# Performance work log

Measured on AMD Instinct MI355X. Metric: run time of the kernel, lower is better.

The kernel has to match this reference:

```python
import jax, jax.numpy as jnp
import numpy as np

X_DIM = 512
HID = 1024


def setup_inputs() -> dict:
    key = jax.random.key(0)
    ks = jax.random.split(key, 9)
    X = jax.random.normal(ks[0], (64, 512, X_DIM), dtype=jnp.float32)
    def w(k, shape):
        return jax.random.normal(k, shape, dtype=jnp.float32) * 0.1
    return {
        "X": X,
        "W_hi": w(ks[1], (HID, HID)), "W_xi": w(ks[2], (X_DIM, HID)), "b_i": jnp.zeros((HID,), jnp.float32),
        "W_hf": w(ks[3], (HID, HID)), "W_xf": w(ks[4], (X_DIM, HID)), "b_f": jnp.zeros((HID,), jnp.float32),
        "W_ho": w(ks[5], (HID, HID)), "W_xo": w(ks[6], (X_DIM, HID)), "b_o": jnp.zeros((HID,), jnp.float32),
        "W_hz": w(ks[7], (HID, HID)), "W_xz": w(ks[8], (X_DIM, HID)), "b_z": jnp.zeros((HID,), jnp.float32),
    }


def reference(X, W_hi, W_xi, b_i, W_hf, W_xf, b_f, W_ho, W_xo, b_o, W_hz, W_xz, b_z):
    B, T, _ = X.shape
    H = W_hi.shape[0]
    # Precompute input projections for all timesteps in one batched GEMM each
    # (same math as per-step x @ W_x*): [B,T,4H]
    Wx = jnp.concatenate([W_xi, W_xf, W_xo, W_xz], axis=1)   # [x_dim, 4H]
    Wh = jnp.concatenate([W_hi, W_hf, W_ho, W_hz], axis=1)   # [H, 4H]
    b = jnp.concatenate([b_i, b_f, b_o, b_z])                # [4H]
    xproj = jnp.einsum('btd,dg->btg', X, Wx) + b             # [B,T,4H]

    def step(carry, xp):
        h, c = carry
        g = h @ Wh + xp                                      # [B,4H]
        i = jax.nn.sigmoid(g[:, 0*H:1*H])
        f = jax.nn.sigmoid(g[:, 1*H:2*H])
        o = jax.nn.sigmoid(g[:, 2*H:3*H])
        z = jnp.tanh(g[:, 3*H:4*H])
        c = i * z + f * c
        h = o * jnp.tanh(c)
        return (h, c), h

    h0 = jnp.zeros((B, H), X.dtype)
    c0 = jnp.zeros((B, H), X.dtype)
    _, hs = jax.lax.scan(step, (h0, c0), jnp.swapaxes(xproj, 0, 1))  # hs: [T,B,H]
    return jnp.swapaxes(hs, 0, 1)                            # [B,T,H]
```

## Files before the change

### kernel.cpp

```cpp
#include <hip/hip_runtime.h>

#define TT 512
#define XD 512
#define HH 1024
#define NGROUP 4
#define BLK_PER_G 64
#define MROWS 16

#define GRP_DW 8192

typedef __attribute__((ext_vector_type(8))) _Float16 h8;
typedef __attribute__((ext_vector_type(4))) float f4;

__global__ __launch_bounds__(256, 1) void lstm_fused(
    const float* __restrict__ X,
    const float* __restrict__ Whi, const float* __restrict__ Wxi, const float* __restrict__ bi_p,
    const float* __restrict__ Whf, const float* __restrict__ Wxf, const float* __restrict__ bf_p,
    const float* __restrict__ Who, const float* __restrict__ Wxo, const float* __restrict__ bo_p,
    const float* __restrict__ Whz, const float* __restrict__ Wxz, const float* __restrict__ bz_p,
    float* __restrict__ out,
    int* __restrict__ flags,
    int* __restrict__ hxch)
{
    __shared__ float red[3][4][2][64][2];
    __shared__ _Float16 sh16[16][16];

    const int tid  = threadIdx.x;
    const int wave = tid >> 6;
    const int lane = tid & 63;
    const int ln   = lane & 15;
    const int lq   = lane >> 4;

    const int blk = blockIdx.x;
    const int g   = blk & 3;
    const int j   = blk >> 2;
    const int colbase = j * 16;
    const int rowbase = g * MROWS;
    const int col = colbase + ln;

    const float* Wh[4]   = {Whi, Whf, Who, Whz};
    const float* Wx[4]   = {Wxi, Wxf, Wxo, Wxz};
    const float* bias[4] = {bi_p, bf_p, bo_p, bz_p};

    h8 bh[4][8];
    h8 bx[4][4];
#pragma unroll
    for (int gi = 0; gi < 4; ++gi) {
        const float* W = Wh[gi];
#pragma unroll
        for (int kt = 0; kt < 8; ++kt) {
            const int k0 = wave * 256 + kt * 32 + lq * 8;
            h8 f;
#pragma unroll
            for (int q = 0; q < 8; ++q) f[q] = (_Float16)W[(k0 + q) * HH + col];
            bh[gi][kt] = f;
        }
        const float* Wq = Wx[gi];
#pragma unroll
        for (int kt = 0; kt < 4; ++kt) {
            const int k0 = wave * 128 + kt * 32 + lq * 8;
            h8 f;
#pragma unroll
            for (int q = 0; q < 8; ++q) f[q] = (_Float16)Wq[(k0 + q) * HH + col];
            bx[gi][kt] = f;
        }
    }
    float bsum[4];
#pragma unroll
    for (int gi = 0; gi < 4; ++gi) bsum[gi] = bias[gi][col];

    float cprev[4] = {0.f, 0.f, 0.f, 0.f};

    const float* Xrow = X + (size_t)(rowbase + ln) * (TT * XD);
    const int xbase = g * GRP_DW;

    for (int t = 0; t < TT; ++t) {
        h8 ax[4];
#pragma unroll
        for (int kt = 0; kt < 4; ++kt) {
            const float4* xp = (const float4*)(Xrow + t * XD + wave * 128 + kt * 32 + lq * 8);
            float4 a = xp[0], b2 = xp[1];
            h8 f;
            f[0] = (_Float16)a.x;  f[1] = (_Float16)a.y;
            f[2] = (_Float16)a.z;  f[3] = (_Float16)a.w;
            f[4] = (_Float16)b2.x; f[5] = (_Float16)b2.y;
            f[6] = (_Float16)b2.z; f[7] = (_Float16)b2.w;
            ax[kt] = f;
        }

        f4 acc[4];
#pragma unroll
        for (int gi = 0; gi < 4; ++gi) acc[gi] = (f4){0.f, 0.f, 0.f, 0.f};

#pragma unroll
        for (int kt = 0; kt < 4; ++kt)
#pragma unroll
            for (int gi = 0; gi < 4; ++gi)
                acc[gi] = __builtin_amdgcn_mfma_f32_16x16x32_f16(ax[kt], bx[gi][kt], acc[gi], 0, 0, 0);

        if (t > 0) {
            int* fl = flags + g * BLK_PER_G;
            while (true) {
                int v = __hip_atomic_load(fl + lane, __ATOMIC_RELAXED, __HIP_MEMORY_SCOPE_AGENT);
                if (__all(v >= t)) break;
                __builtin_amdgcn_s_sleep(1);
            }
            asm volatile("" ::: "memory");

            const int rb = ((t - 1) & 1) * (NGROUP * GRP_DW) + xbase;
            h8 ah[8];
#pragma unroll
            for (int kt = 0; kt < 8; ++kt) {
                const int dwi = rb + ((wave * 32 + kt * 4 + lq) * 16 + ln) * 4;
                union { int i[4]; h8 f; } u;
                u.i[0] = __hip_atomic_load(hxch + dwi + 0, __ATOMIC_RELAXED, __HIP_MEMORY_SCOPE_AGENT);
                u.i[1] = __hip_atomic_load(hxch + dwi + 1, __ATOMIC_RELAXED, __HIP_MEMORY_SCOPE_AGENT);
                u.i[2] = __hip_atomic_load(hxch + dwi + 2, __ATOMIC_RELAXED, __HIP_MEMORY_SCOPE_AGENT);
                u.i[3] = __hip_atomic_load(hxch + dwi + 3, __ATOMIC_RELAXED, __HIP_MEMORY_SCOPE_AGENT);
                ah[kt] = u.f;
            }
#pragma unroll
            for (int kt = 0; kt < 8; ++kt)
#pragma unroll
                for (int gi = 0; gi < 4; ++gi)
                    acc[gi] = __builtin_amdgcn_mfma_f32_16x16x32_f16(ah[kt], bh[gi][kt], acc[gi], 0, 0, 0);
        }

        if (wave > 0) {
#pragma unroll
            for (int gi = 0; gi < 4; ++gi) {
                red[wave - 1][gi][0][lane][0] = acc[gi][0];
                red[wave - 1][gi][0][lane][1] = acc[gi][1];
                red[wave - 1][gi][1][lane][0] = acc[gi][2];
                red[wave - 1][gi][1][lane][1] = acc[gi][3];
            }
        }
        __syncthreads();

        if (wave == 0) {
#pragma unroll
            for (int w = 0; w < 3; ++w)
#pragma unroll
                for (int gi = 0; gi < 4; ++gi) {
                    acc[gi][0] += red[w][gi][0][lane][0];
                    acc[gi][1] += red[w][gi][0][lane][1];
                    acc[gi][2] += red[w][gi][1][lane][0];
                    acc[gi][3] += red[w][gi][1][lane][1];
                }

#pragma unroll
            for (int r = 0; r < 4; ++r) {
                float gi_ = acc[0][r] + bsum[0];
                float gf_ = acc[1][r] + bsum[1];
                float go_ = acc[2][r] + bsum[2];
                float gz_ = acc[3][r] + bsum[3];
                float i_ = 1.f / (1.f + __expf(-gi_));
                float f_ = 1.f / (1.f + __expf(-gf_));
                float o_ = 1.f / (1.f + __expf(-go_));
                float z_ = 1.f - 2.f / (__expf(2.f * gz_) + 1.f);
                float c_ = i_ * z_ + f_ * cprev[r];
                cprev[r] = c_;
                float h_ = o_ * (1.f - 2.f / (__expf(2.f * c_) + 1.f));
                const int m = lq * 4 + r;
                out[(size_t)(rowbase + m) * (TT * HH) + (size_t)t * HH + col] = h_;
                sh16[m][ln] = (_Float16)h_;
            }

            asm volatile("s_waitcnt lgkmcnt(0)" ::: "memory");
            if (lane < 32) {
                const int prow = lane & 15;
                const int pk8  = lane >> 4;
                const int4 pk = *(const int4*)&sh16[prow][pk8 * 8];
                const int wb = (t & 1) * (NGROUP * GRP_DW) + xbase
                             + ((j * 2 + pk8) * 16 + prow) * 4;
                __hip_atomic_store(hxch + wb + 0, pk.x, __ATOMIC_RELAXED, __HIP_MEMORY_SCOPE_AGENT);
                __hip_atomic_store(hxch + wb + 1, pk.y, __ATOMIC_RELAXED, __HIP_MEMORY_SCOPE_AGENT);
                __hip_atomic_store(hxch + wb + 2, pk.z, __ATOMIC_RELAXED, __HIP_MEMORY_SCOPE_AGENT);
                __hip_atomic_store(hxch + wb + 3, pk.w, __ATOMIC_RELAXED, __HIP_MEMORY_SCOPE_AGENT);
            }
            asm volatile("s_waitcnt vmcnt(0)" ::: "memory");
            if (lane == 0) {
                __hip_atomic_store(&flags[g * BLK_PER_G + j], t + 1,
                                   __ATOMIC_RELAXED, __HIP_MEMORY_SCOPE_AGENT);
            }
        }
    }
}

extern "C" void kernel_launch(void* const* d_in, const int* in_sizes, int n_in,
                              void* d_out, int out_size, void* d_ws, size_t ws_size,
                              hipStream_t stream) {
    const float* X   = (const float*)d_in[0];
    const float* Whi = (const float*)d_in[1];
    const float* Wxi = (const float*)d_in[2];
    const float* bi  = (const float*)d_in[3];
    const float* Whf = (const float*)d_in[4];
    const float* Wxf = (const float*)d_in[5];
    const float* bf  = (const float*)d_in[6];
    const float* Who = (const float*)d_in[7];
    const float* Wxo = (const float*)d_in[8];
    const float* bo  = (const float*)d_in[9];
    const float* Whz = (const float*)d_in[10];
    const float* Wxz = (const float*)d_in[11];
    const float* bz  = (const float*)d_in[12];
    float* out = (float*)d_out;

    int* flags = (int*)d_ws;
    int* hxch  = flags + 256;
    hipMemsetAsync(d_ws, 0, NGROUP * BLK_PER_G * sizeof(int), stream);

    lstm_fused<<<dim3(256), dim3(256), 0, stream>>>(
        X, Whi, Wxi, bi, Whf, Wxf, bf, Who, Wxo, bo, Whz, Wxz, bz, out, flags, hxch);
}
```

Measured before the change: 3.084 ms.

## Split LSTM gate epilogue across two waves and prefetch next-step X inputs

Moves the flag poll and h-exchange loads to the start of each step, so the X-projection MFMAs no longer sit on the critical path after the wait. The next step's X rows are prefetched into registers during the current step. The gate reduction and activations are split across two waves, with a shared-memory token so that all h stores finish before the flag is published. Exchange loads and stores are widened to 64-bit atomics and each wave polls only 16 flags. The cost is an LDS spin between waves and more registers held for prefetched data.

Result: slower. 3.838 ms (+24.4%).

```diff
diff --git a/kernel.cpp b/kernel.cpp
--- a/kernel.cpp
+++ b/kernel.cpp
@@ -5,12 +5,15 @@
 #define HH 1024
 #define NGROUP 4
 #define BLK_PER_G 64
-#define MROWS 16
-
 #define GRP_DW 8192
 
 typedef __attribute__((ext_vector_type(8))) _Float16 h8;
 typedef __attribute__((ext_vector_type(4))) float f4;
+typedef __attribute__((ext_vector_type(4))) int i4;
+typedef unsigned long long u64;
+
+__device__ __forceinline__ float sigf(float x) { return 1.f / (1.f + __expf(-x)); }
+__device__ __forceinline__ float tanhfast(float x) { return 1.f - 2.f / (__expf(2.f * x) + 1.f); }
 
 __global__ __launch_bounds__(256, 1) void lstm_fused(
     const float* __restrict__ X,
@@ -22,8 +25,9 @@
     int* __restrict__ flags,
     int* __restrict__ hxch)
 {
-    __shared__ float red[3][4][2][64][2];
-    __shared__ _Float16 sh16[16][16];
+    __shared__ f4 red[4][4][64];
+    __shared__ __align__(16) _Float16 sh16[16][16];
+    __shared__ int stoken;
 
     const int tid  = threadIdx.x;
     const int wave = tid >> 6;
@@ -35,8 +39,10 @@
     const int g   = blk & 3;
     const int j   = blk >> 2;
     const int colbase = j * 16;
-    const int rowbase = g * MROWS;
+    const int rowbase = g * 16;
     const int col = colbase + ln;
+
+    if (tid == 0) stoken = 0;
 
     const float* Wh[4]   = {Whi, Whf, Who, Whz};
     const float* Wx[4]   = {Wxi, Wxf, Wxo, Wxz};
@@ -69,17 +75,52 @@
 #pragma unroll
     for (int gi = 0; gi < 4; ++gi) bsum[gi] = bias[gi][col];
 
-    float cprev[4] = {0.f, 0.f, 0.f, 0.f};
+    const int m0 = (wave & 1) * 8 + lq * 2;
+    const int m1 = m0 + 1;
+    float cp0 = 0.f, cp1 = 0.f;
 
     const float* Xrow = X + (size_t)(rowbase + ln) * (TT * XD);
-    const int xbase = g * GRP_DW;
+    const int gbase = g * GRP_DW;
+
+    const int* fp = flags + g * BLK_PER_G + ((lane < 16) ? (wave * 16 + lane) : j);
+
+    float4 xv[8];
+    {
+        const float* xb = Xrow + wave * 128;
+#pragma unroll
+        for (int kt = 0; kt < 4; ++kt) {
+            const float4* xp = (const float4*)(xb + kt * 32 + lq * 8);
+            xv[2 * kt] = xp[0]; xv[2 * kt + 1] = xp[1];
+        }
+    }
+    __syncthreads();
+
+    u64 hv[8][2];
 
     for (int t = 0; t < TT; ++t) {
+        if (t > 0) {
+            while (true) {
+                int v = __hip_atomic_load(fp, __ATOMIC_RELAXED, __HIP_MEMORY_SCOPE_AGENT);
+                if (__all(v >= t)) break;
+                __builtin_amdgcn_s_sleep(1);
+            }
+            const int rb = ((t - 1) & 1) * (NGROUP * GRP_DW) + gbase;
+#pragma unroll
+            for (int kt = 0; kt < 8; ++kt) {
+                const u64* hp = (const u64*)(hxch + rb + ((wave * 32 + kt * 4 + lq) * 16 + ln) * 4);
+                hv[kt][0] = __hip_atomic_load(hp + 0, __ATOMIC_RELAXED, __HIP_MEMORY_SCOPE_AGENT);
+                hv[kt][1] = __hip_atomic_load(hp + 1, __ATOMIC_RELAXED, __HIP_MEMORY_SCOPE_AGENT);
+            }
+        }
+
+        f4 acc[4];
+#pragma unroll
+        for (int gi = 0; gi < 4; ++gi) acc[gi] = (f4){0.f, 0.f, 0.f, 0.f};
+
         h8 ax[4];
 #pragma unroll
         for (int kt = 0; kt < 4; ++kt) {
-            const float4* xp = (const float4*)(Xrow + t * XD + wave * 128 + kt * 32 + lq * 8);
-            float4 a = xp[0], b2 = xp[1];
+            float4 a = xv[2 * kt], b2 = xv[2 * kt + 1];
             h8 f;
             f[0] = (_Float16)a.x;  f[1] = (_Float16)a.y;
             f[2] = (_Float16)a.z;  f[3] = (_Float16)a.w;
@@ -87,11 +128,6 @@
             f[6] = (_Float16)b2.z; f[7] = (_Float16)b2.w;
             ax[kt] = f;
         }
-
-        f4 acc[4];
-#pragma unroll
-        for (int gi = 0; gi < 4; ++gi) acc[gi] = (f4){0.f, 0.f, 0.f, 0.f};
-
 #pragma unroll
         for (int kt = 0; kt < 4; ++kt)
 #pragma unroll
@@ -99,89 +135,87 @@
                 acc[gi] = __builtin_amdgcn_mfma_f32_16x16x32_f16(ax[kt], bx[gi][kt], acc[gi], 0, 0, 0);
 
         if (t > 0) {
-            int* fl = flags + g * BLK_PER_G;
-            while (true) {
-                int v = __hip_atomic_load(fl + lane, __ATOMIC_RELAXED, __HIP_MEMORY_SCOPE_AGENT);
-                if (__all(v >= t)) break;
-                __builtin_amdgcn_s_sleep(1);
+#pragma unroll
+            for (int kt = 0; kt < 8; ++kt) {
+                union { u64 u[2]; h8 f; } uu;
+                uu.u[0] = hv[kt][0]; uu.u[1] = hv[kt][1];
+#pragma unroll
+                for (int gi = 0; gi < 4; ++gi)
+                    acc[gi] = __builtin_amdgcn_mfma_f32_16x16x32_f16(uu.f, bh[gi][kt], acc[gi], 0, 0, 0);
+            }
+        }
+
+#pragma unroll
+        for (int gi = 0; gi < 4; ++gi) red[wave][gi][lane] = acc[gi];
+
+        if (wave >= 2 && t < TT - 1) {
+            const float* xb = Xrow + (t + 1) * XD + wave * 128;
+#pragma unroll
+            for (int kt = 0; kt < 4; ++kt) {
+                const float4* xp = (const float4*)(xb + kt * 32 + lq * 8);
+                xv[2 * kt] = xp[0]; xv[2 * kt + 1] = xp[1];
+            }
+        }
+        __syncthreads();
+
+        if (wave < 2) {
+            const int lqp = m0 >> 2;
+            const int sl  = lqp * 16 + ln;
+            const int e0  = m0 & 3;
+            float ga[4], gb[4];
+#pragma unroll
+            for (int gi = 0; gi < 4; ++gi) {
+                float s0 = bsum[gi], s1 = bsum[gi];
+#pragma unroll
+                for (int wv = 0; wv < 4; ++wv) {
+                    const float* rp = (const float*)&red[wv][gi][sl];
+                    float2 p = *(const float2*)(rp + e0);
+                    s0 += p.x; s1 += p.y;
+                }
+                ga[gi] = s0; gb[gi] = s1;
+            }
+            float i0 = sigf(ga[0]), f0 = sigf(ga[1]), o0 = sigf(ga[2]), z0 = tanhfast(ga[3]);
+            float c0 = i0 * z0 + f0 * cp0; cp0 = c0;
+            float h0 = o0 * tanhfast(c0);
+            float i1 = sigf(gb[0]), f1 = sigf(gb[1]), o1 = sigf(gb[2]), z1 = tanhfast(gb[3]);
+            float c1 = i1 * z1 + f1 * cp1; cp1 = c1;
+            float h1 = o1 * tanhfast(c1);
+
+            sh16[m0][ln] = (_Float16)h0;
+            sh16[m1][ln] = (_Float16)h1;
+
+            asm volatile("s_waitcnt lgkmcnt(0)" ::: "memory");
+            if (lane < 16) {
+                const int half2 = lane >> 3;
+                const int row   = (wave & 1) * 8 + (lane & 7);
+                i4 pk = *(const i4*)&sh16[row][half2 * 8];
+                int* wp = hxch + (t & 1) * (NGROUP * GRP_DW) + gbase
+                        + ((2 * j + half2) * 16 + row) * 4;
+                union { i4 v; u64 u[2]; } pu; pu.v = pk;
+                __hip_atomic_store((u64*)wp,     pu.u[0], __ATOMIC_RELAXED, __HIP_MEMORY_SCOPE_AGENT);
+                __hip_atomic_store((u64*)wp + 1, pu.u[1], __ATOMIC_RELAXED, __HIP_MEMORY_SCOPE_AGENT);
+            }
+            asm volatile("s_waitcnt vmcnt(0)" ::: "memory");
+            if (wave == 0) {
+                *(volatile int*)&stoken = t + 1;
+            } else {
+                while (*(volatile int*)&stoken < t + 1) {}
+                if (lane == 0)
+                    __hip_atomic_store(&flags[g * BLK_PER_G + j], t + 1,
+                                       __ATOMIC_RELAXED, __HIP_MEMORY_SCOPE_AGENT);
             }
             asm volatile("" ::: "memory");
 
-            const int rb = ((t - 1) & 1) * (NGROUP * GRP_DW) + xbase;
-            h8 ah[8];
-#pragma unroll
-            for (int kt = 0; kt < 8; ++kt) {
-                const int dwi = rb + ((wave * 32 + kt * 4 + lq) * 16 + ln) * 4;
-                union { int i[4]; h8 f; } u;
-                u.i[0] = __hip_atomic_load(hxch + dwi + 0, __ATOMIC_RELAXED, __HIP_MEMORY_SCOPE_AGENT);
-                u.i[1] = __hip_atomic_load(hxch + dwi + 1, __ATOMIC_RELAXED, __HIP_MEMORY_SCOPE_AGENT);
-                u.i[2] = __hip_atomic_load(hxch + dwi + 2, __ATOMIC_RELAXED, __HIP_MEMORY_SCOPE_AGENT);
-                u.i[3] = __hip_atomic_load(hxch + dwi + 3, __ATOMIC_RELAXED, __HIP_MEMORY_SCOPE_AGENT);
-                ah[kt] = u.f;
-            }
-#pragma unroll
-            for (int kt = 0; kt < 8; ++kt)
-#pragma unroll
-                for (int gi = 0; gi < 4; ++gi)
-                    acc[gi] = __builtin_amdgcn_mfma_f32_16x16x32_f16(ah[kt], bh[gi][kt], acc[gi], 0, 0, 0);
-        }
-
-        if (wave > 0) {
-#pragma unroll
-            for (int gi = 0; gi < 4; ++gi) {
-                red[wave - 1][gi][0][lane][0] = acc[gi][0];
-                red[wave - 1][gi][0][lane][1] = acc[gi][1];
-                red[wave - 1][gi][1][lane][0] = acc[gi][2];
-                red[wave - 1][gi][1][lane][1] = acc[gi][3];
-            }
-        }
-        __syncthreads();
-
-        if (wave == 0) {
-#pragma unroll
-            for (int w = 0; w < 3; ++w)
-#pragma unroll
-                for (int gi = 0; gi < 4; ++gi) {
-                    acc[gi][0] += red[w][gi][0][lane][0];
-                    acc[gi][1] += red[w][gi][0][lane][1];
-                    acc[gi][2] += red[w][gi][1][lane][0];
-                    acc[gi][3] += red[w][gi][1][lane][1];
+            out[(size_t)(rowbase + m0) * (TT * HH) + (size_t)t * HH + col] = h0;
+            out[(size_t)(rowbase + m1) * (TT * HH) + (size_t)t * HH + col] = h1;
+
+            if (t < TT - 1) {
+                const float* xb = Xrow + (t + 1) * XD + wave * 128;
+#pragma unroll
+                for (int kt = 0; kt < 4; ++kt) {
+                    const float4* xp = (const float4*)(xb + kt * 32 + lq * 8);
+                    xv[2 * kt] = xp[0]; xv[2 * kt + 1] = xp[1];
                 }
-
-#pragma unroll
-            for (int r = 0; r < 4; ++r) {
-                float gi_ = acc[0][r] + bsum[0];
-                float gf_ = acc[1][r] + bsum[1];
-                float go_ = acc[2][r] + bsum[2];
-                float gz_ = acc[3][r] + bsum[3];
-                float i_ = 1.f / (1.f + __expf(-gi_));
-                float f_ = 1.f / (1.f + __expf(-gf_));
-                float o_ = 1.f / (1.f + __expf(-go_));
-                float z_ = 1.f - 2.f / (__expf(2.f * gz_) + 1.f);
-                float c_ = i_ * z_ + f_ * cprev[r];
-                cprev[r] = c_;
-                float h_ = o_ * (1.f - 2.f / (__expf(2.f * c_) + 1.f));
-                const int m = lq * 4 + r;
-                out[(size_t)(rowbase + m) * (TT * HH) + (size_t)t * HH + col] = h_;
-                sh16[m][ln] = (_Float16)h_;
-            }
-
-            asm volatile("s_waitcnt lgkmcnt(0)" ::: "memory");
-            if (lane < 32) {
-                const int prow = lane & 15;
-                const int pk8  = lane >> 4;
-                const int4 pk = *(const int4*)&sh16[prow][pk8 * 8];
-                const int wb = (t & 1) * (NGROUP * GRP_DW) + xbase
-                             + ((j * 2 + pk8) * 16 + prow) * 4;
-                __hip_atomic_store(hxch + wb + 0, pk.x, __ATOMIC_RELAXED, __HIP_MEMORY_SCOPE_AGENT);
-                __hip_atomic_store(hxch + wb + 1, pk.y, __ATOMIC_RELAXED, __HIP_MEMORY_SCOPE_AGENT);
-                __hip_atomic_store(hxch + wb + 2, pk.z, __ATOMIC_RELAXED, __HIP_MEMORY_SCOPE_AGENT);
-                __hip_atomic_store(hxch + wb + 3, pk.w, __ATOMIC_RELAXED, __HIP_MEMORY_SCOPE_AGENT);
-            }
-            asm volatile("s_waitcnt vmcnt(0)" ::: "memory");
-            if (lane == 0) {
-                __hip_atomic_store(&flags[g * BLK_PER_G + j], t + 1,
-                                   __ATOMIC_RELAXED, __HIP_MEMORY_SCOPE_AGENT);
             }
         }
     }
```
